# Kernel tuning notes

Hardware: AMD Instinct MI355X
Metric: run time of the kernel (lower is better)

Reference implementation:

```python
import jax, jax.numpy as jnp
import numpy as np

B, S, D = 2, 2048, 1024
NH, NKV = 16, 4
HD = D // NH          # 64
NREP = NH // NKV      # 4
E, TOPK = 8, 2
CAP_FACTOR = 1.25
HID = 4 * D // 3      # 1365 (hardcoded in MoELayer)
EPS = 1e-6


def rmsnorm(x, w):
    xf = x.astype(jnp.float32)
    y = xf * jax.lax.rsqrt(jnp.mean(xf * xf, axis=-1, keepdims=True) + EPS)
    return y.astype(x.dtype) * w


def apply_rope(x, cos, sin):
    # x: [b, s, h, hd]; cos/sin: [1, s, 1, hd]
    half = x.shape[-1] // 2
    x1, x2 = x[..., :half], x[..., half:]
    ch, sh = cos[..., :half], sin[..., :half]
    return jnp.concatenate([x1 * ch - x2 * sh, x1 * sh + x2 * ch], axis=-1)


def swiglu(x, w1, w2, w3):
    return (jax.nn.silu(x @ w1) * (x @ w3)) @ w2


def setup_inputs():
    key = jax.random.key(0)
    ks = jax.random.split(key, 14)
    x = jax.random.normal(ks[0], (B, S, D), jnp.float32)
    # RoPE tables (standard 10000 base), duplicated halves so cos[..., :half] is valid
    pos = jnp.arange(S, dtype=jnp.float32)[:, None]
    inv = 1.0 / (10000.0 ** (jnp.arange(0, HD, 2, dtype=jnp.float32) / HD))  # [HD/2]
    ang = pos * inv[None, :]                                                # [S, HD/2]
    cos = jnp.concatenate([jnp.cos(ang), jnp.cos(ang)], -1)[None, :, None, :]
    sin = jnp.concatenate([jnp.sin(ang), jnp.sin(ang)], -1)[None, :, None, :]
    # causal additive mask [1,1,S,S]
    causal = jnp.tril(jnp.ones((S, S), bool))
    mask = jnp.where(causal, 0.0, -1e9).astype(jnp.float32)[None, None]
    s = 0.02
    return {
        'x': x, 'cos': cos, 'sin': sin, 'mask': mask,
        'attn_norm_w': jnp.ones((D,), jnp.float32),
        'moe_norm_w': jnp.ones((D,), jnp.float32),
        'wq': jax.random.normal(ks[1], (D, NH * HD), jnp.float32) * s,
        'wk': jax.random.normal(ks[2], (D, NKV * HD), jnp.float32) * s,
        'wv': jax.random.normal(ks[3], (D, NKV * HD), jnp.float32) * s,
        'wo': jax.random.normal(ks[4], (NH * HD, D), jnp.float32) * s,
        'router_w': jax.random.normal(ks[5], (D, E), jnp.float32) * s,
        'ew1': jax.random.normal(ks[6], (E, D, HID), jnp.float32) * s,
        'ew2': jax.random.normal(ks[7], (E, HID, D), jnp.float32) * s,
        'ew3': jax.random.normal(ks[8], (E, D, HID), jnp.float32) * s,
        'sw1': jax.random.normal(ks[9], (D, HID), jnp.float32) * s,
        'sw2': jax.random.normal(ks[10], (HID, D), jnp.float32) * s,
        'sw3': jax.random.normal(ks[11], (D, HID), jnp.float32) * s,
    }


def reference(x, cos, sin, mask, attn_norm_w, moe_norm_w, wq, wk, wv, wo,
              router_w, ew1, ew2, ew3, sw1, sw2, sw3):
    # ---- attention path ----
    xn = rmsnorm(x, attn_norm_w)
    q = (xn @ wq).reshape(B, S, NH, HD)
    k = (xn @ wk).reshape(B, S, NKV, HD)
    v = (xn @ wv).reshape(B, S, NKV, HD)
    q = apply_rope(q, cos, sin)
    k = apply_rope(k, cos, sin)
    new_k, new_v = k, v  # kv cache outputs (no prior cache)
    # repeat_interleave kv heads to NH
    k_rep = jnp.repeat(k, NREP, axis=2)  # [b,s,NH,hd]
    v_rep = jnp.repeat(v, NREP, axis=2)
    scores = jnp.einsum('bqhd,bkhd->bhqk', q, k_rep) / np.sqrt(HD)
    scores = scores + mask[:, :, -S:, :]
    attn = jax.nn.softmax(scores.astype(jnp.float32), axis=-1).astype(q.dtype)
    ao = jnp.einsum('bhqk,bkhd->bqhd', attn, v_rep).reshape(B, S, NH * HD)
    h = x + ao @ wo

    # ---- MoE path ----
    hn = rmsnorm(h, moe_norm_w)
    x_flat = hn.reshape(-1, D)            # [T, D]
    T = x_flat.shape[0]
    logits = x_flat @ router_w            # [T, E]
    probs = jax.nn.softmax(logits, axis=-1)
    w_topk, idx = jax.lax.top_k(probs, TOPK)          # [T, K]
    w_topk = w_topk / jnp.sum(w_topk, axis=-1, keepdims=True)
    onehot = jax.nn.one_hot(idx, E, dtype=jnp.float32)  # [T, K, E]
    counts = jnp.sum(onehot, axis=(0, 1))               # [E]
    util = jnp.mean((counts > 0).astype(jnp.float32)) * 100.0
    fraction = counts / T
    aux_loss = E * jnp.sum(jnp.mean(probs, axis=0) * fraction)
    capacity = int(T * TOPK / E * CAP_FACTOR)
    member = jnp.sum(onehot, axis=1) > 0                 # [T, E] token assigned to expert
    keep = member & (jnp.cumsum(member.astype(jnp.int32), axis=0) <= capacity)
    gate = jnp.sum(w_topk[:, :, None] * onehot, axis=1)  # [T, E] combine weights
    gate = gate * keep.astype(gate.dtype)
    # dense per-expert SwiGLU (same math as masked dispatch; zero-gated tokens vanish)
    h1 = jnp.einsum('td,edh->eth', x_flat, ew1)
    h3 = jnp.einsum('td,edh->eth', x_flat, ew3)
    eo = jnp.einsum('eth,ehd->etd', jax.nn.silu(h1) * h3, ew2)
    moe_out = jnp.einsum('etd,te->td', eo, gate).reshape(B, S, D)
    moe_out = moe_out + swiglu(hn, sw1, sw2, sw3)  # shared expert

    out = h + moe_out
    return out, aux_loss, util, new_k, new_v
```

## Files before the change

kernel.cpp:

```cpp
#include <hip/hip_runtime.h>
#include <hip/hip_bf16.h>
#include <math.h>

typedef __hip_bfloat16 bf16;
typedef __attribute__((ext_vector_type(8))) short short8;
typedef __attribute__((ext_vector_type(4))) float floatx4;

#define SEQ    2048
#define TTOK   4096
#define DM     1024
#define NHEAD  16
#define NKVH   4
#define HD     64
#define NEXP   8
#define HIDDEN 1365
#define HIDP   1408
#define CAPT   1280
#define NSLOT  (NEXP*CAPT)
#define TSLOT  (NSLOT+TTOK)
#define XPE    (CAPT/128)
#define XBT    14

__device__ __forceinline__ void gld16(const void* g, void* l) {
  __builtin_amdgcn_global_load_lds((const __attribute__((address_space(1))) void*)g,
                                   (__attribute__((address_space(3))) void*)l,
                                   16, 0, 0);
}

struct __align__(8) bf4 { bf16 x, y, z, w; };

struct EpiAux {
  const float* cosb; const float* sinb;
  bf16* qb; bf16* kb; bf16* vb; float* newk; float* newv;
};

__global__ __launch_bounds__(256) void transpose_cvt(
    const float* __restrict__ src, bf16* __restrict__ dst,
    int K, int N, int Kp, long srcZ, long dstZ) {
  src += (size_t)blockIdx.z * srcZ;
  dst += (size_t)blockIdx.z * dstZ;
  __shared__ float tile[64][65];
  const int tid = threadIdx.x;
  const int k0 = blockIdx.y * 64, n0 = blockIdx.x * 64;
  const int lr = tid >> 4, lc = (tid & 15) * 4;
#pragma unroll
  for (int i = 0; i < 4; ++i) {
    int k = k0 + lr + i * 16;
    int n = n0 + lc;
    float4 v = {0.f, 0.f, 0.f, 0.f};
    if (k < K) {
      if (n + 3 < N) v = *(const float4*)(src + (size_t)k * N + n);
      else {
        float* vp = (float*)&v;
        for (int e = 0; e < 4; ++e) if (n + e < N) vp[e] = src[(size_t)k * N + n + e];
      }
    }
    tile[lr + i * 16][lc] = v.x; tile[lr + i * 16][lc + 1] = v.y;
    tile[lr + i * 16][lc + 2] = v.z; tile[lr + i * 16][lc + 3] = v.w;
  }
  __syncthreads();
  const int n = tid >> 2, kk0 = (tid & 3) * 16;
  if (n0 + n < N) {
    bf16 buf[16];
#pragma unroll
    for (int e = 0; e < 16; ++e) buf[e] = (bf16)tile[kk0 + e][n];
    bf16* dp = dst + (size_t)(n0 + n) * Kp + k0 + kk0;
    *(short8*)dp = *(short8*)buf;
    *(short8*)(dp + 8) = *(short8*)(buf + 8);
  }
}

__global__ __launch_bounds__(256) void rmsnorm_kernel(
    const float* __restrict__ x, const float* __restrict__ w, bf16* __restrict__ out) {
  int t = blockIdx.x;
  const float* xr = x + (size_t)t * DM;
  float4 xv = *(const float4*)(xr + threadIdx.x * 4);
  float ss = xv.x * xv.x + xv.y * xv.y + xv.z * xv.z + xv.w * xv.w;
#pragma unroll
  for (int off = 1; off < 64; off <<= 1) ss += __shfl_xor(ss, off);
  __shared__ float sred[4];
  if ((threadIdx.x & 63) == 0) sred[threadIdx.x >> 6] = ss;
  __syncthreads();
  float scale = rsqrtf((sred[0] + sred[1] + sred[2] + sred[3]) * (1.f / DM) + 1e-6f);
  float4 wv = *(const float4*)(w + threadIdx.x * 4);
  bf4 o;
  o.x = (bf16)(xv.x * scale * wv.x); o.y = (bf16)(xv.y * scale * wv.y);
  o.z = (bf16)(xv.z * scale * wv.z); o.w = (bf16)(xv.w * scale * wv.w);
  ((bf4*)(out + (size_t)t * DM))[threadIdx.x] = o;
}

__global__ __launch_bounds__(256) void rmsnorm_router_kernel(
    const float* __restrict__ x, const float* __restrict__ w, const float* __restrict__ rw,
    bf16* __restrict__ out, float* __restrict__ probs,
    int* __restrict__ tIdx, float* __restrict__ tW) {
  int t = blockIdx.x;
  int tid = threadIdx.x, lane = tid & 63, wv = tid >> 6;
  const float* xr = x + (size_t)t * DM;
  float4 xv = *(const float4*)(xr + tid * 4);
  float ss = xv.x * xv.x + xv.y * xv.y + xv.z * xv.z + xv.w * xv.w;
#pragma unroll
  for (int off = 1; off < 64; off <<= 1) ss += __shfl_xor(ss, off);
  __shared__ float sred[4];
  __shared__ float red[4][8];
  if (lane == 0) sred[wv] = ss;
  __syncthreads();
  float scale = rsqrtf((sred[0] + sred[1] + sred[2] + sred[3]) * (1.f / DM) + 1e-6f);
  float4 wvv = *(const float4*)(w + tid * 4);
  float y[4] = {xv.x * scale * wvv.x, xv.y * scale * wvv.y,
                xv.z * scale * wvv.z, xv.w * scale * wvv.w};
  bf4 o; o.x = (bf16)y[0]; o.y = (bf16)y[1]; o.z = (bf16)y[2]; o.w = (bf16)y[3];
  ((bf4*)(out + (size_t)t * DM))[tid] = o;
  float acc[8] = {0, 0, 0, 0, 0, 0, 0, 0};
#pragma unroll
  for (int dd = 0; dd < 4; ++dd) {
    const float* rwr = rw + (size_t)(tid * 4 + dd) * 8;
#pragma unroll
    for (int e = 0; e < 8; ++e) acc[e] += y[dd] * rwr[e];
  }
#pragma unroll
  for (int e = 0; e < 8; ++e)
#pragma unroll
    for (int off = 1; off < 64; off <<= 1) acc[e] += __shfl_xor(acc[e], off);
  if (lane == 0)
#pragma unroll
    for (int e = 0; e < 8; ++e) red[wv][e] = acc[e];
  __syncthreads();
  if (tid == 0) {
    float lg[8];
#pragma unroll
    for (int e = 0; e < 8; ++e) lg[e] = red[0][e] + red[1][e] + red[2][e] + red[3][e];
    float mx = lg[0];
#pragma unroll
    for (int e = 1; e < 8; ++e) mx = fmaxf(mx, lg[e]);
    float p[8], se = 0.f;
#pragma unroll
    for (int e = 0; e < 8; ++e) { p[e] = __expf(lg[e] - mx); se += p[e]; }
#pragma unroll
    for (int e = 0; e < 8; ++e) { p[e] /= se; probs[t * 8 + e] = p[e]; }
    int i1 = 0;
#pragma unroll
    for (int e = 1; e < 8; ++e) if (p[e] > p[i1]) i1 = e;
    int i2 = (i1 == 0) ? 1 : 0;
#pragma unroll
    for (int e = 0; e < 8; ++e) if (e != i1 && p[e] > p[i2]) i2 = e;
    float s = p[i1] + p[i2];
    tIdx[t * 2] = i1; tIdx[t * 2 + 1] = i2;
    tW[t * 2] = p[i1] / s; tW[t * 2 + 1] = p[i2] / s;
  }
}

template <int EPI>
__global__ __launch_bounds__(256) void gemm_bt(
    const bf16* __restrict__ A, const bf16* __restrict__ Bt,
    int M, int N, int K, int lda, int ldb, int xPerXcd,
    float* __restrict__ Cf, int ldc,
    const float* __restrict__ resid, EpiAux aux) {
  __shared__ __align__(16) bf16 As[64 * 64];
  __shared__ __align__(16) bf16 Bs[128 * 64];
  const int tid = threadIdx.x, lane = tid & 63, wave = tid >> 6;
  const int f = blockIdx.x, lo = f >> 3;
  int xb = (f & 7) * xPerXcd + lo % xPerXcd;
  int n0 = (lo / xPerXcd) * 128;
  int m0 = xb * 64;

  const bf16* aSrc[2]; const bf16* bSrc[4];
  bf16* aDst[2]; bf16* bDst[4];
#pragma unroll
  for (int it = 0; it < 2; ++it) {
    int c = it * 256 + tid;
    int r = c >> 3, q = c & 7;
    int kq = q ^ (r & 7);
    aSrc[it] = A + (long)(m0 + r) * lda + kq * 8;
    aDst[it] = As + (size_t)(it * 256 + wave * 64) * 8;
  }
#pragma unroll
  for (int it = 0; it < 4; ++it) {
    int c = it * 256 + tid;
    int r = c >> 3, q = c & 7;
    int kq = q ^ (r & 7);
    bSrc[it] = Bt + (long)(n0 + r) * ldb + kq * 8;
    bDst[it] = Bs + (size_t)(it * 256 + wave * 64) * 8;
  }

  floatx4 acc[2][4];
#pragma unroll
  for (int i = 0; i < 2; ++i)
#pragma unroll
    for (int j = 0; j < 4; ++j) { floatx4 z = {0.f, 0.f, 0.f, 0.f}; acc[i][j] = z; }

  const int wm = (wave & 1) * 32, wn = (wave >> 1) * 64;
  const int l15 = lane & 15, quad = lane >> 4;
  int aOff[2][2], bOff[4][2];
#pragma unroll
  for (int h = 0; h < 2; ++h) {
#pragma unroll
    for (int i = 0; i < 2; ++i) {
      int m = wm + i * 16 + l15;
      aOff[i][h] = (((m << 3) | ((h * 4 + quad) ^ (m & 7))) << 3);
    }
#pragma unroll
    for (int j = 0; j < 4; ++j) {
      int n = wn + j * 16 + l15;
      bOff[j][h] = (((n << 3) | ((h * 4 + quad) ^ (n & 7))) << 3);
    }
  }

  const int kIters = K >> 6;
  for (int kt = 0; kt < kIters; ++kt) {
    __syncthreads();
#pragma unroll
    for (int it = 0; it < 2; ++it) { gld16(aSrc[it], aDst[it]); aSrc[it] += 64; }
#pragma unroll
    for (int it = 0; it < 4; ++it) { gld16(bSrc[it], bDst[it]); bSrc[it] += 64; }
    __syncthreads();
#pragma unroll
    for (int h = 0; h < 2; ++h) {
      short8 af[2], bfr[4];
#pragma unroll
      for (int i = 0; i < 2; ++i) af[i] = *(const short8*)(As + aOff[i][h]);
#pragma unroll
      for (int j = 0; j < 4; ++j) bfr[j] = *(const short8*)(Bs + bOff[j][h]);
#pragma unroll
      for (int i = 0; i < 2; ++i)
#pragma unroll
        for (int j = 0; j < 4; ++j)
          acc[i][j] = __builtin_amdgcn_mfma_f32_16x16x32_bf16(af[i], bfr[j], acc[i][j], 0, 0, 0);
    }
  }

  if constexpr (EPI == 4) {
#pragma unroll
    for (int i = 0; i < 2; ++i) {
#pragma unroll
      for (int r = 0; r < 4; ++r) {
        int row = wm + i * 16 + quad * 4 + r;
        int t = m0 + row;
        int s = t & (SEQ - 1);
        if (n0 < 1024) {
#pragma unroll
          for (int j = 0; j < 2; ++j) {
            int col = n0 + wn + j * 16 + l15;
            int dlo = col & 63;
            float x1 = acc[i][j][r], x2 = acc[i][j + 2][r];
            float ch = aux.cosb[s * 64 + dlo], sh = aux.sinb[s * 64 + dlo];
            aux.qb[(size_t)t * DM + col]      = (bf16)((x1 * ch - x2 * sh) * 0.125f);
            aux.qb[(size_t)t * DM + col + 32] = (bf16)((x1 * sh + x2 * ch) * 0.125f);
          }
        } else if (n0 < 1280) {
#pragma unroll
          for (int j = 0; j < 2; ++j) {
            int ck = n0 + wn + j * 16 + l15 - 1024;
            int dlo = ck & 63;
            float x1 = acc[i][j][r], x2 = acc[i][j + 2][r];
            float ch = aux.cosb[s * 64 + dlo], sh = aux.sinb[s * 64 + dlo];
            float o1 = x1 * ch - x2 * sh, o2 = x1 * sh + x2 * ch;
            aux.kb[(size_t)t * 256 + ck]        = (bf16)o1;
            aux.kb[(size_t)t * 256 + ck + 32]   = (bf16)o2;
            aux.newk[(size_t)t * 256 + ck]      = o1;
            aux.newk[(size_t)t * 256 + ck + 32] = o2;
          }
        } else {
#pragma unroll
          for (int j = 0; j < 4; ++j) {
            int cv = n0 + wn + j * 16 + l15 - 1280;
            float v = acc[i][j][r];
            aux.vb[(size_t)t * 256 + cv]   = (bf16)v;
            aux.newv[(size_t)t * 256 + cv] = v;
          }
        }
      }
    }
    return;
  }
#pragma unroll
  for (int i = 0; i < 2; ++i) {
#pragma unroll
    for (int j = 0; j < 4; ++j) {
      int col = n0 + wn + j * 16 + l15;
#pragma unroll
      for (int r = 0; r < 4; ++r) {
        int row = wm + i * 16 + quad * 4 + r;
        size_t o = (size_t)(m0 + row) * ldc + col;
        Cf[o] = resid[o] + acc[i][j][r];
      }
    }
  }
}

__device__ __forceinline__ bool slot_block(
    int f, int NY, const int* neCnt, int& expert, int& m0, int& mLimit, int& n0) {
  int xcd = f & 7, lo = f >> 3;
  int xb = lo / NY, y = lo % NY;
  n0 = y * 64;
  if (xb < XPE) {
    expert = xcd;
    int ne = neCnt[xcd];
    if (xb * 128 >= ne) return false;
    m0 = xcd * CAPT + xb * 128;
    mLimit = ne - xb * 128;
    if (mLimit > 128) mLimit = 128;
  } else {
    expert = 8;
    int sb = xcd * 4 + (xb - XPE);
    m0 = NSLOT + sb * 128;
    mLimit = 128;
  }
  return true;
}

__global__ __launch_bounds__(256, 2) void gemm_dual9(
    const bf16* __restrict__ A, const bf16* __restrict__ B1t, const bf16* __restrict__ B3t,
    bf16* __restrict__ mact,
    const int* __restrict__ tokList, const int* __restrict__ neCnt) {
  __shared__ __align__(16) bf16 As[128 * 64];
  __shared__ __align__(16) bf16 B1s[128 * 64];
  __shared__ __align__(16) bf16 B3s[128 * 64];
  const int tid = threadIdx.x, lane = tid & 63, wave = tid >> 6;
  int expert, m0, mLimit, n0;
  if (!slot_block(blockIdx.x, 11, neCnt, expert, m0, mLimit, n0)) return;
  n0 <<= 1;
  const bf16* B1e = B1t + (long)expert * (HIDDEN * 1024);
  const bf16* B3e = B3t + (long)expert * (HIDDEN * 1024);

  const bf16* aSrc[4]; const bf16* b1Src[4]; const bf16* b3Src[4];
  bf16* aDst[4]; bf16* b1Dst[4]; bf16* b3Dst[4];
#pragma unroll
  for (int it = 0; it < 4; ++it) {
    int c = it * 256 + tid;
    int r = c >> 3, q = c & 7;
    int kq = q ^ (r & 7);
    int rr = r < mLimit ? r : (mLimit - 1);
    aSrc[it] = A + (long)tokList[m0 + rr] * 1024 + kq * 8;
    aDst[it] = As + (size_t)(it * 256 + wave * 64) * 8;
    int nn = n0 + r; if (nn > HIDDEN - 1) nn = HIDDEN - 1;
    b1Src[it] = B1e + (long)nn * 1024 + kq * 8;
    b3Src[it] = B3e + (long)nn * 1024 + kq * 8;
    b1Dst[it] = B1s + (size_t)(it * 256 + wave * 64) * 8;
    b3Dst[it] = B3s + (size_t)(it * 256 + wave * 64) * 8;
  }

  floatx4 acc1[4][4], acc3[4][4];
#pragma unroll
  for (int i = 0; i < 4; ++i)
#pragma unroll
    for (int j = 0; j < 4; ++j) {
      floatx4 z = {0.f, 0.f, 0.f, 0.f};
      acc1[i][j] = z; acc3[i][j] = z;
    }

  const int wm = (wave & 1) * 64, wn = (wave >> 1) * 64;
  const int l15 = lane & 15, quad = lane >> 4;
  int aOff[4][2], bOff[4][2];
#pragma unroll
  for (int h = 0; h < 2; ++h) {
#pragma unroll
    for (int i = 0; i < 4; ++i) {
      int m = wm + i * 16 + l15;
      aOff[i][h] = (((m << 3) | ((h * 4 + quad) ^ (m & 7))) << 3);
    }
#pragma unroll
    for (int j = 0; j < 4; ++j) {
      int n = wn + j * 16 + l15;
      bOff[j][h] = (((n << 3) | ((h * 4 + quad) ^ (n & 7))) << 3);
    }
  }

  for (int kt = 0; kt < 16; ++kt) {
    __syncthreads();
#pragma unroll
    for (int it = 0; it < 4; ++it) { gld16(aSrc[it], aDst[it]); aSrc[it] += 64; }
#pragma unroll
    for (int it = 0; it < 4; ++it) {
      gld16(b1Src[it], b1Dst[it]); b1Src[it] += 64;
      gld16(b3Src[it], b3Dst[it]); b3Src[it] += 64;
    }
    __syncthreads();
#pragma unroll
    for (int h = 0; h < 2; ++h) {
      short8 af[4];
#pragma unroll
      for (int i = 0; i < 4; ++i) af[i] = *(const short8*)(As + aOff[i][h]);
#pragma unroll
      for (int j = 0; j < 4; ++j) {
        short8 b1f = *(const short8*)(B1s + bOff[j][h]);
        short8 b3f = *(const short8*)(B3s + bOff[j][h]);
#pragma unroll
        for (int i = 0; i < 4; ++i) {
          acc1[i][j] = __builtin_amdgcn_mfma_f32_16x16x32_bf16(af[i], b1f, acc1[i][j], 0, 0, 0);
          acc3[i][j] = __builtin_amdgcn_mfma_f32_16x16x32_bf16(af[i], b3f, acc3[i][j], 0, 0, 0);
        }
      }
    }
  }

#pragma unroll
  for (int i = 0; i < 4; ++i) {
#pragma unroll
    for (int j = 0; j < 4; ++j) {
      int col = n0 + wn + j * 16 + l15;
#pragma unroll
      for (int r = 0; r < 4; ++r) {
        int row = wm + i * 16 + quad * 4 + r;
        if (row >= mLimit) continue;
        float a1 = acc1[i][j][r], a3 = acc3[i][j][r];
        float sl = a1 / (1.f + __expf(-a1));
        mact[(size_t)(m0 + row) * HIDP + col] = (col < HIDDEN) ? (bf16)(sl * a3) : (bf16)0.f;
      }
    }
  }
}

__global__ __launch_bounds__(256) void gemm_down9(
    const bf16* __restrict__ A, const bf16* __restrict__ B2t,
    bf16* __restrict__ eo,
    const float* __restrict__ gateW, const int* __restrict__ neCnt) {
  __shared__ __align__(16) bf16 As[128 * 64];
  __shared__ __align__(16) bf16 Bs[64 * 64];
  const int tid = threadIdx.x, lane = tid & 63, wave = tid >> 6;
  int expert, m0, mLimit, n0;
  if (!slot_block(blockIdx.x, 16, neCnt, expert, m0, mLimit, n0)) return;
  const bf16* Be = B2t + (long)expert * (1024 * HIDP);

  const bf16* aSrc[4]; const bf16* bSrc[2];
  bf16* aDst[4]; bf16* bDst[2];
#pragma unroll
  for (int it = 0; it < 4; ++it) {
    int c = it * 256 + tid;
    int r = c >> 3, q = c & 7;
    int kq = q ^ (r & 7);
    int rr = r < mLimit ? r : (mLimit - 1);
    aSrc[it] = A + (long)(m0 + rr) * HIDP + kq * 8;
    aDst[it] = As + (size_t)(it * 256 + wave * 64) * 8;
  }
#pragma unroll
  for (int it = 0; it < 2; ++it) {
    int c = it * 256 + tid;
    int r = c >> 3, q = c & 7;
    int kq = q ^ (r & 7);
    bSrc[it] = Be + (long)(n0 + r) * HIDP + kq * 8;
    bDst[it] = Bs + (size_t)(it * 256 + wave * 64) * 8;
  }

  floatx4 acc[4][2];
#pragma unroll
  for (int i = 0; i < 4; ++i)
#pragma unroll
    for (int j = 0; j < 2; ++j) { floatx4 z = {0.f, 0.f, 0.f, 0.f}; acc[i][j] = z; }

  const int wm = (wave & 1) * 64, wn = (wave >> 1) * 32;
  const int l15 = lane & 15, quad = lane >> 4;
  int aOff[4][2], bOff[2][2];
#pragma unroll
  for (int h = 0; h < 2; ++h) {
#pragma unroll
    for (int i = 0; i < 4; ++i) {
      int m = wm + i * 16 + l15;
      aOff[i][h] = (((m << 3) | ((h * 4 + quad) ^ (m & 7))) << 3);
    }
#pragma unroll
    for (int j = 0; j < 2; ++j) {
      int n = wn + j * 16 + l15;
      bOff[j][h] = (((n << 3) | ((h * 4 + quad) ^ (n & 7))) << 3);
    }
  }

  for (int kt = 0; kt < 22; ++kt) {
    __syncthreads();
#pragma unroll
    for (int it = 0; it < 4; ++it) { gld16(aSrc[it], aDst[it]); aSrc[it] += 64; }
#pragma unroll
    for (int it = 0; it < 2; ++it) { gld16(bSrc[it], bDst[it]); bSrc[it] += 64; }
    __syncthreads();
#pragma unroll
    for (int h = 0; h < 2; ++h) {
      short8 af[4];
#pragma unroll
      for (int i = 0; i < 4; ++i) af[i] = *(const short8*)(As + aOff[i][h]);
#pragma unroll
      for (int j = 0; j < 2; ++j) {
        short8 bf = *(const short8*)(Bs + bOff[j][h]);
#pragma unroll
        for (int i = 0; i < 4; ++i)
          acc[i][j] = __builtin_amdgcn_mfma_f32_16x16x32_bf16(af[i], bf, acc[i][j], 0, 0, 0);
      }
    }
  }

#pragma unroll
  for (int i = 0; i < 4; ++i) {
#pragma unroll
    for (int j = 0; j < 2; ++j) {
      int col = n0 + wn + j * 16 + l15;
#pragma unroll
      for (int r = 0; r < 4; ++r) {
        int row = wm + i * 16 + quad * 4 + r;
        if (row >= mLimit) continue;
        eo[(size_t)(m0 + row) * 1024 + col] = (bf16)(gateW[m0 + row] * acc[i][j][r]);
      }
    }
  }
}

__global__ __launch_bounds__(256) void vt_kernel(
    const bf16* __restrict__ vb, bf16* __restrict__ vt) {
  __shared__ __align__(16) bf16 tile[64 * 72];
  int t0 = blockIdx.x * 64, bg = blockIdx.y;
  int b = bg >> 2, g = bg & 3;
  int tid = threadIdx.x;
  for (int c = tid; c < 512; c += 256) {
    int r = c >> 3, d8 = (c & 7) * 8;
    *(short8*)(tile + r * 72 + d8) =
        *(const short8*)(vb + (size_t)(b * SEQ + t0 + r) * 256 + g * 64 + d8);
  }
  __syncthreads();
  for (int c = tid; c < 512; c += 256) {
    int d = c >> 3, s8 = (c & 7) * 8;
    bf16 tmp[8];
#pragma unroll
    for (int x = 0; x < 8; ++x) tmp[x] = tile[(s8 + x) * 72 + d];
    *(short8*)(vt + ((size_t)bg * 64 + d) * SEQ + t0 + s8) = *(short8*)tmp;
  }
}

__global__ __launch_bounds__(256) void attn_kernel(
    const bf16* __restrict__ Q, const bf16* __restrict__ Kc, const bf16* __restrict__ Vt,
    bf16* __restrict__ AO) {
  __shared__ __align__(16) bf16 Qs[64 * 64];
  __shared__ __align__(16) bf16 Ks[64 * 64];
  __shared__ __align__(16) bf16 Vs[64 * 64];
  __shared__ __align__(16) bf16 Ps[4][16 * 64];
  const int pairI = blockIdx.x, h = blockIdx.y, b = blockIdx.z;
  const int g = h >> 2;
  const int tid = threadIdx.x, lane = tid & 63, wave = tid >> 6;
  const int l15 = lane & 15, quad = lane >> 4;

  const bf16* kSrc[2]; const bf16* vSrc[2]; bf16* kDst[2]; bf16* vDst[2];
#pragma unroll
  for (int it = 0; it < 2; ++it) {
    int c = it * 256 + tid;
    int r = c >> 3, p = c & 7;
    int kq = p ^ (r & 7);
    kSrc[it] = Kc + (size_t)(b * SEQ + r) * 256 + g * 64 + kq * 8;
    vSrc[it] = Vt + ((size_t)(b * 4 + g) * 64 + r) * SEQ + kq * 8;
    kDst[it] = Ks + (size_t)(it * 256 + wave * 64) * 8;
    vDst[it] = Vs + (size_t)(it * 256 + wave * 64) * 8;
  }

  int qOff[2], kvOff[4][2], pOff[2];
#pragma unroll
  for (int hh = 0; hh < 2; ++hh) {
    int m = wave * 16 + l15;
    qOff[hh] = (m << 6) + (((hh * 4 + quad) ^ (m & 7)) << 3);
#pragma unroll
    for (int j = 0; j < 4; ++j) {
      int n = j * 16 + l15;
      kvOff[j][hh] = (n << 6) + (((hh * 4 + quad) ^ (n & 7)) << 3);
    }
    int cblk = (hh * 2 + (quad >> 1)) ^ (l15 >> 2);
    pOff[hh] = (l15 << 6) + (cblk << 4) + ((quad & 1) << 3);
  }
  bf16* pw = &Ps[wave][0];
  const int rowl = wave * 16 + quad * 4;

  short8 onesb;
#pragma unroll
  for (int e = 0; e < 8; ++e) onesb[e] = (short)0x3F80;

  for (int ph = 0; ph < 2; ++ph) {
    const int q0 = (ph == 0 ? pairI : 31 - pairI) * 64;
    __syncthreads();
#pragma unroll
    for (int it = 0; it < 2; ++it) {
      int c = it * 256 + tid;
      int r = c >> 3, p = c & 7;
      int kq = p ^ (r & 7);
      gld16(Q + (size_t)(b * SEQ + q0 + r) * DM + h * 64 + kq * 8,
            Qs + (size_t)(it * 256 + wave * 64) * 8);
    }

    floatx4 oacc[4], sumacc;
#pragma unroll
    for (int r = 0; r < 4; ++r) { floatx4 z = {0.f, 0.f, 0.f, 0.f}; oacc[r] = z; }
    { floatx4 z = {0.f, 0.f, 0.f, 0.f}; sumacc = z; }

    const int nkt = (q0 >> 6) + 1;
    for (int kt = 0; kt < nkt; ++kt) {
      __syncthreads();
#pragma unroll
      for (int it = 0; it < 2; ++it) {
        gld16(kSrc[it] + (size_t)kt * 64 * 256, kDst[it]);
        gld16(vSrc[it] + kt * 64, vDst[it]);
      }
      __syncthreads();

      floatx4 sacc[4];
#pragma unroll
      for (int j = 0; j < 4; ++j) { floatx4 z = {0.f, 0.f, 0.f, 0.f}; sacc[j] = z; }
#pragma unroll
      for (int hh = 0; hh < 2; ++hh) {
        short8 aq = *(const short8*)(Qs + qOff[hh]);
#pragma unroll
        for (int j = 0; j < 4; ++j)
          sacc[j] = __builtin_amdgcn_mfma_f32_16x16x32_bf16(
              aq, *(const short8*)(Ks + kvOff[j][hh]), sacc[j], 0, 0, 0);
      }

      const bool lastTile = (kt == nkt - 1);
#pragma unroll
      for (int j = 0; j < 4; ++j) {
        int sw = ((j ^ quad) << 4) + l15;
        int colg = j * 16 + l15;
#pragma unroll
        for (int r = 0; r < 4; ++r) {
          float p = __expf(sacc[j][r]);
          if (lastTile && colg > rowl + r) p = 0.f;
          pw[(quad * 4 + r) * 64 + sw] = (bf16)p;
        }
      }
      asm volatile("s_waitcnt lgkmcnt(0)" ::: "memory");
#pragma unroll
      for (int hh = 0; hh < 2; ++hh) {
        short8 ap = *(const short8*)(pw + pOff[hh]);
#pragma unroll
        for (int j = 0; j < 4; ++j)
          oacc[j] = __builtin_amdgcn_mfma_f32_16x16x32_bf16(
              ap, *(const short8*)(Vs + kvOff[j][hh]), oacc[j], 0, 0, 0);
        sumacc = __builtin_amdgcn_mfma_f32_16x16x32_bf16(ap, onesb, sumacc, 0, 0, 0);
      }
    }

    float inv[4];
#pragma unroll
    for (int r = 0; r < 4; ++r) inv[r] = 1.f / sumacc[r];
#pragma unroll
    for (int j = 0; j < 4; ++j)
#pragma unroll
      for (int r = 0; r < 4; ++r) {
        int t = b * SEQ + q0 + rowl + r;
        AO[(size_t)t * DM + h * 64 + j * 16 + l15] = (bf16)(oacc[j][r] * inv[r]);
      }
  }
}

__global__ __launch_bounds__(256) void assign_kernel(
    const int* __restrict__ tIdx, const float* __restrict__ tW,
    int* __restrict__ tokList, float* __restrict__ gateW,
    int* __restrict__ neCnt, int* __restrict__ cntFull, int* __restrict__ slotOf) {
  int e = blockIdx.x;
  int tid = threadIdx.x, lane = tid & 63, wv = tid >> 6;
  if (e == 8) {
    for (int t = tid; t < TTOK; t += 256) {
      tokList[NSLOT + t] = t;
      gateW[NSLOT + t] = 1.0f;
    }
    if (tid == 0) neCnt[8] = TTOK;
    return;
  }
  __shared__ int waveTot[4];
  __shared__ int offs;
  if (tid == 0) offs = 0;
  __syncthreads();
  for (int base = 0; base < TTOK; base += 256) {
    int t = base + tid;
    int a = tIdx[t * 2], b2 = tIdx[t * 2 + 1];
    bool sel = (a == e) || (b2 == e);
    unsigned long long mask = __ballot(sel);
    int wrank = __popcll(mask & ((1ull << lane) - 1ull));
    if (lane == 0) waveTot[wv] = __popcll(mask);
    __syncthreads();
    int pre = offs;
    for (int w2 = 0; w2 < wv; ++w2) pre += waveTot[w2];
    int rank = pre + wrank;
    if (sel && rank < CAPT) {
      int slot = e * CAPT + rank;
      tokList[slot] = t;
      gateW[slot] = (a == e) ? tW[t * 2] : tW[t * 2 + 1];
      slotOf[t * 2 + ((a == e) ? 0 : 1)] = slot;
    }
    __syncthreads();
    if (tid == 0) offs += waveTot[0] + waveTot[1] + waveTot[2] + waveTot[3];
    __syncthreads();
  }
  if (tid == 0) {
    cntFull[e] = offs;
    neCnt[e] = offs < CAPT ? offs : CAPT;
  }
}

__global__ __launch_bounds__(256) void aux_kernel(
    const float* __restrict__ probs, const int* __restrict__ cntFull,
    float* __restrict__ outAux) {
  __shared__ float psum[8];
  if (threadIdx.x < 8) psum[threadIdx.x] = 0.f;
  __syncthreads();
  float lp[8] = {0, 0, 0, 0, 0, 0, 0, 0};
  for (int t = threadIdx.x; t < TTOK; t += 256) {
#pragma unroll
    for (int e = 0; e < 8; ++e) lp[e] += probs[t * 8 + e];
  }
#pragma unroll
  for (int e = 0; e < 8; ++e)
#pragma unroll
    for (int off = 1; off < 64; off <<= 1) lp[e] += __shfl_xor(lp[e], off);
  if ((threadIdx.x & 63) == 0)
#pragma unroll
    for (int e = 0; e < 8; ++e) atomicAdd(&psum[e], lp[e]);
  __syncthreads();
  if (threadIdx.x == 0) {
    float aux = 0.f; int used = 0;
    for (int e = 0; e < 8; ++e) {
      aux += (psum[e] / (float)TTOK) * ((float)cntFull[e] / (float)TTOK);
      if (cntFull[e] > 0) used++;
    }
    outAux[0] = 8.f * aux;
    outAux[1] = 100.f * (float)used / 8.f;
  }
}

__global__ __launch_bounds__(256) void combine_kernel(
    float* __restrict__ outp, const float* __restrict__ hbuf,
    const bf16* __restrict__ eo, const int* __restrict__ slotOf) {
  int t = blockIdx.x, tid = threadIdx.x;
  float4 v = ((const float4*)(hbuf + (size_t)t * DM))[tid];
  bf4 sh = ((const bf4*)(eo + (size_t)(NSLOT + t) * DM))[tid];
  v.x += (float)sh.x; v.y += (float)sh.y; v.z += (float)sh.z; v.w += (float)sh.w;
  int s0 = slotOf[t * 2], s1 = slotOf[t * 2 + 1];
  if (s0 >= 0) {
    bf4 e = ((const bf4*)(eo + (size_t)s0 * DM))[tid];
    v.x += (float)e.x; v.y += (float)e.y; v.z += (float)e.z; v.w += (float)e.w;
  }
  if (s1 >= 0) {
    bf4 e = ((const bf4*)(eo + (size_t)s1 * DM))[tid];
    v.x += (float)e.x; v.y += (float)e.y; v.z += (float)e.z; v.w += (float)e.w;
  }
  ((float4*)(outp + (size_t)t * DM))[tid] = v;
}

extern "C" void kernel_launch(void* const* d_in, const int* in_sizes, int n_in,
                              void* d_out, int out_size, void* d_ws, size_t ws_size,
                              hipStream_t stream) {
  (void)in_sizes; (void)n_in; (void)out_size; (void)ws_size;
  const float* x     = (const float*)d_in[0];
  const float* cosb  = (const float*)d_in[1];
  const float* sinb  = (const float*)d_in[2];
  const float* attnw = (const float*)d_in[4];
  const float* moew  = (const float*)d_in[5];
  const float* wq  = (const float*)d_in[6];
  const float* wk  = (const float*)d_in[7];
  const float* wv  = (const float*)d_in[8];
  const float* wo  = (const float*)d_in[9];
  const float* rw  = (const float*)d_in[10];
  const float* ew1 = (const float*)d_in[11];
  const float* ew2 = (const float*)d_in[12];
  const float* ew3 = (const float*)d_in[13];
  const float* sw1 = (const float*)d_in[14];
  const float* sw2 = (const float*)d_in[15];
  const float* sw3 = (const float*)d_in[16];

  float* outp = (float*)d_out;
  float* auxp = outp + 4194304;
  float* newk = outp + 4194306;
  float* newv = newk + 1048576;

  char* wsp = (char*)d_ws;
  size_t off = 0;
  auto alloc = [&](size_t bytes) -> void* {
    void* p = wsp + off; off += (bytes + 255) & ~(size_t)255; return p;
  };
  bf16* wqkvT = (bf16*)alloc((size_t)1536 * 1024 * 2);
  bf16* woT   = (bf16*)alloc((size_t)1024 * 1024 * 2);
  bf16* ew1T  = (bf16*)alloc((size_t)9 * HIDDEN * 1024 * 2);
  bf16* ew3T  = (bf16*)alloc((size_t)9 * HIDDEN * 1024 * 2);
  bf16* ew2T  = (bf16*)alloc((size_t)9 * 1024 * HIDP * 2);
  bf16* xn    = (bf16*)alloc((size_t)TTOK * DM * 2);
  bf16* qb    = (bf16*)alloc((size_t)TTOK * DM * 2);
  bf16* kb    = (bf16*)alloc((size_t)TTOK * 256 * 2);
  bf16* vb    = (bf16*)alloc((size_t)TTOK * 256 * 2);
  bf16* vt    = (bf16*)alloc((size_t)TTOK * 256 * 2);
  bf16* ao    = (bf16*)alloc((size_t)TTOK * DM * 2);
  float* hbuf = (float*)alloc((size_t)TTOK * DM * 4);
  bf16* hn    = (bf16*)alloc((size_t)TTOK * DM * 2);
  float* probs = (float*)alloc((size_t)TTOK * 8 * 4);
  int*   tIdx  = (int*)alloc((size_t)TTOK * 2 * 4);
  float* tW    = (float*)alloc((size_t)TTOK * 2 * 4);
  int*   tokList = (int*)alloc((size_t)TSLOT * 4);
  float* gateW   = (float*)alloc((size_t)TSLOT * 4);
  int*   neCnt   = (int*)alloc(64);
  int*   cntFull = (int*)alloc(64);
  int*   slotOf  = (int*)alloc((size_t)TTOK * 2 * 4);
  bf16*  mact = (bf16*)alloc((size_t)TSLOT * HIDP * 2);
  bf16*  eo   = (bf16*)alloc((size_t)TSLOT * DM * 2);

  EpiAux nil{};
  EpiAux ropeAux{cosb, sinb, qb, kb, vb, newk, newv};

  transpose_cvt<<<dim3(16, 16, 1), 256, 0, stream>>>(wq, wqkvT, 1024, 1024, 1024, 0, 0);
  transpose_cvt<<<dim3(4, 16, 1), 256, 0, stream>>>(wk, wqkvT + (size_t)1024 * 1024, 1024, 256, 1024, 0, 0);
  transpose_cvt<<<dim3(4, 16, 1), 256, 0, stream>>>(wv, wqkvT + (size_t)1280 * 1024, 1024, 256, 1024, 0, 0);
  transpose_cvt<<<dim3(16, 16, 1), 256, 0, stream>>>(wo, woT, 1024, 1024, 1024, 0, 0);
  transpose_cvt<<<dim3(22, 16, NEXP), 256, 0, stream>>>(ew1, ew1T, 1024, HIDDEN, 1024,
      (long)1024 * HIDDEN, (long)HIDDEN * 1024);
  transpose_cvt<<<dim3(22, 16, NEXP), 256, 0, stream>>>(ew3, ew3T, 1024, HIDDEN, 1024,
      (long)1024 * HIDDEN, (long)HIDDEN * 1024);
  transpose_cvt<<<dim3(16, 22, NEXP), 256, 0, stream>>>(ew2, ew2T, HIDDEN, 1024, HIDP,
      (long)HIDDEN * 1024, (long)1024 * HIDP);
  transpose_cvt<<<dim3(22, 16, 1), 256, 0, stream>>>(sw1, ew1T + (size_t)8 * HIDDEN * 1024,
      1024, HIDDEN, 1024, 0, 0);
  transpose_cvt<<<dim3(22, 16, 1), 256, 0, stream>>>(sw3, ew3T + (size_t)8 * HIDDEN * 1024,
      1024, HIDDEN, 1024, 0, 0);
  transpose_cvt<<<dim3(16, 22, 1), 256, 0, stream>>>(sw2, ew2T + (size_t)8 * 1024 * HIDP,
      HIDDEN, 1024, HIDP, 0, 0);

  rmsnorm_kernel<<<TTOK, 256, 0, stream>>>(x, attnw, xn);
  gemm_bt<4><<<8 * 8 * 12, 256, 0, stream>>>(
      xn, wqkvT, TTOK, 1536, 1024, 1024, 1024, 8, nullptr, 0, nullptr, ropeAux);
  vt_kernel<<<dim3(32, 8), 256, 0, stream>>>(vb, vt);
  attn_kernel<<<dim3(16, NHEAD, 2), 256, 0, stream>>>(qb, kb, vt, ao);
  gemm_bt<2><<<8 * 8 * 8, 256, 0, stream>>>(
      ao, woT, TTOK, 1024, 1024, 1024, 1024, 8, hbuf, 1024, x, nil);

  rmsnorm_router_kernel<<<TTOK, 256, 0, stream>>>(hbuf, moew, rw, hn, probs, tIdx, tW);
  hipMemsetAsync(slotOf, 0xFF, (size_t)TTOK * 2 * 4, stream);
  assign_kernel<<<9, 256, 0, stream>>>(tIdx, tW, tokList, gateW, neCnt, cntFull, slotOf);
  aux_kernel<<<1, 256, 0, stream>>>(probs, cntFull, auxp);

  gemm_dual9<<<8 * XBT * 11, 256, 0, stream>>>(hn, ew1T, ew3T, mact, tokList, neCnt);
  gemm_down9<<<8 * XBT * 16, 256, 0, stream>>>(mact, ew2T, eo, gateW, neCnt);
  combine_kernel<<<TTOK, 256, 0, stream>>>(outp, hbuf, eo, slotOf);
}
```

Before: 560.9 us.

## Fuse MoE combine into down-projection via atomic scatter-add; unpair attention query tiles

The down-projection GEMM now scatters gate-weighted results straight into the output with float atomicAdd, keyed by each slot's token. The output projection writes the residual sum into the output buffer as well. This removes the eo intermediate buffer, the slotOf map with its memset, and the combine kernel. Separately, attention launches one block per 64-row query tile, heaviest first, instead of pairing a light and a heavy tile in one block. Atomics make the summation order nondeterministic and add contention on the output.

```diff
diff --git a/kernel.cpp b/kernel.cpp
--- a/kernel.cpp
+++ b/kernel.cpp
@@ -154,7 +154,7 @@
     const bf16* __restrict__ A, const bf16* __restrict__ Bt,
     int M, int N, int K, int lda, int ldb, int xPerXcd,
     float* __restrict__ Cf, int ldc,
-    const float* __restrict__ resid, EpiAux aux) {
+    const float* __restrict__ resid, float* __restrict__ out2, EpiAux aux) {
   __shared__ __align__(16) bf16 As[64 * 64];
   __shared__ __align__(16) bf16 Bs[128 * 64];
   const int tid = threadIdx.x, lane = tid & 63, wave = tid >> 6;
@@ -281,7 +281,9 @@
       for (int r = 0; r < 4; ++r) {
         int row = wm + i * 16 + quad * 4 + r;
         size_t o = (size_t)(m0 + row) * ldc + col;
-        Cf[o] = resid[o] + acc[i][j][r];
+        float v = resid[o] + acc[i][j][r];
+        Cf[o] = v;
+        out2[o] = v;
       }
     }
   }
@@ -412,8 +414,9 @@
 
 __global__ __launch_bounds__(256) void gemm_down9(
     const bf16* __restrict__ A, const bf16* __restrict__ B2t,
-    bf16* __restrict__ eo,
-    const float* __restrict__ gateW, const int* __restrict__ neCnt) {
+    float* __restrict__ outp,
+    const float* __restrict__ gateW, const int* __restrict__ tokList,
+    const int* __restrict__ neCnt) {
   __shared__ __align__(16) bf16 As[128 * 64];
   __shared__ __align__(16) bf16 Bs[64 * 64];
   const int tid = threadIdx.x, lane = tid & 63, wave = tid >> 6;
@@ -489,13 +492,16 @@
 #pragma unroll
   for (int i = 0; i < 4; ++i) {
 #pragma unroll
-    for (int j = 0; j < 2; ++j) {
-      int col = n0 + wn + j * 16 + l15;
-#pragma unroll
-      for (int r = 0; r < 4; ++r) {
-        int row = wm + i * 16 + quad * 4 + r;
-        if (row >= mLimit) continue;
-        eo[(size_t)(m0 + row) * 1024 + col] = (bf16)(gateW[m0 + row] * acc[i][j][r]);
+    for (int r = 0; r < 4; ++r) {
+      int row = wm + i * 16 + quad * 4 + r;
+      if (row >= mLimit) continue;
+      int slot = m0 + row;
+      int tok = tokList[slot];
+      float gw = gateW[slot];
+#pragma unroll
+      for (int j = 0; j < 2; ++j) {
+        int col = n0 + wn + j * 16 + l15;
+        atomicAdd(outp + (size_t)tok * 1024 + col, gw * acc[i][j][r]);
       }
     }
   }
@@ -529,7 +535,8 @@
   __shared__ __align__(16) bf16 Ks[64 * 64];
   __shared__ __align__(16) bf16 Vs[64 * 64];
   __shared__ __align__(16) bf16 Ps[4][16 * 64];
-  const int pairI = blockIdx.x, h = blockIdx.y, b = blockIdx.z;
+  const int h = blockIdx.y, b = blockIdx.z;
+  const int q0 = (31 - blockIdx.x) * 64;
   const int g = h >> 2;
   const int tid = threadIdx.x, lane = tid & 63, wave = tid >> 6;
   const int l15 = lane & 15, quad = lane >> 4;
@@ -566,86 +573,82 @@
 #pragma unroll
   for (int e = 0; e < 8; ++e) onesb[e] = (short)0x3F80;
 
-  for (int ph = 0; ph < 2; ++ph) {
-    const int q0 = (ph == 0 ? pairI : 31 - pairI) * 64;
+#pragma unroll
+  for (int it = 0; it < 2; ++it) {
+    int c = it * 256 + tid;
+    int r = c >> 3, p = c & 7;
+    int kq = p ^ (r & 7);
+    gld16(Q + (size_t)(b * SEQ + q0 + r) * DM + h * 64 + kq * 8,
+          Qs + (size_t)(it * 256 + wave * 64) * 8);
+  }
+
+  floatx4 oacc[4], sumacc;
+#pragma unroll
+  for (int r = 0; r < 4; ++r) { floatx4 z = {0.f, 0.f, 0.f, 0.f}; oacc[r] = z; }
+  { floatx4 z = {0.f, 0.f, 0.f, 0.f}; sumacc = z; }
+
+  const int nkt = (q0 >> 6) + 1;
+  for (int kt = 0; kt < nkt; ++kt) {
     __syncthreads();
 #pragma unroll
     for (int it = 0; it < 2; ++it) {
-      int c = it * 256 + tid;
-      int r = c >> 3, p = c & 7;
-      int kq = p ^ (r & 7);
-      gld16(Q + (size_t)(b * SEQ + q0 + r) * DM + h * 64 + kq * 8,
-            Qs + (size_t)(it * 256 + wave * 64) * 8);
-    }
-
-    floatx4 oacc[4], sumacc;
-#pragma unroll
-    for (int r = 0; r < 4; ++r) { floatx4 z = {0.f, 0.f, 0.f, 0.f}; oacc[r] = z; }
-    { floatx4 z = {0.f, 0.f, 0.f, 0.f}; sumacc = z; }
-
-    const int nkt = (q0 >> 6) + 1;
-    for (int kt = 0; kt < nkt; ++kt) {
-      __syncthreads();
-#pragma unroll
-      for (int it = 0; it < 2; ++it) {
-        gld16(kSrc[it] + (size_t)kt * 64 * 256, kDst[it]);
-        gld16(vSrc[it] + kt * 64, vDst[it]);
+      gld16(kSrc[it] + (size_t)kt * 64 * 256, kDst[it]);
+      gld16(vSrc[it] + kt * 64, vDst[it]);
+    }
+    __syncthreads();
+
+    floatx4 sacc[4];
+#pragma unroll
+    for (int j = 0; j < 4; ++j) { floatx4 z = {0.f, 0.f, 0.f, 0.f}; sacc[j] = z; }
+#pragma unroll
+    for (int hh = 0; hh < 2; ++hh) {
+      short8 aq = *(const short8*)(Qs + qOff[hh]);
+#pragma unroll
+      for (int j = 0; j < 4; ++j)
+        sacc[j] = __builtin_amdgcn_mfma_f32_16x16x32_bf16(
+            aq, *(const short8*)(Ks + kvOff[j][hh]), sacc[j], 0, 0, 0);
+    }
+
+    const bool lastTile = (kt == nkt - 1);
+#pragma unroll
+    for (int j = 0; j < 4; ++j) {
+      int sw = ((j ^ quad) << 4) + l15;
+      int colg = j * 16 + l15;
+#pragma unroll
+      for (int r = 0; r < 4; ++r) {
+        float p = __expf(sacc[j][r]);
+        if (lastTile && colg > rowl + r) p = 0.f;
+        pw[(quad * 4 + r) * 64 + sw] = (bf16)p;
       }
-      __syncthreads();
-
-      floatx4 sacc[4];
-#pragma unroll
-      for (int j = 0; j < 4; ++j) { floatx4 z = {0.f, 0.f, 0.f, 0.f}; sacc[j] = z; }
-#pragma unroll
-      for (int hh = 0; hh < 2; ++hh) {
-        short8 aq = *(const short8*)(Qs + qOff[hh]);
-#pragma unroll
-        for (int j = 0; j < 4; ++j)
-          sacc[j] = __builtin_amdgcn_mfma_f32_16x16x32_bf16(
-              aq, *(const short8*)(Ks + kvOff[j][hh]), sacc[j], 0, 0, 0);
-      }
-
-      const bool lastTile = (kt == nkt - 1);
-#pragma unroll
-      for (int j = 0; j < 4; ++j) {
-        int sw = ((j ^ quad) << 4) + l15;
-        int colg = j * 16 + l15;
-#pragma unroll
-        for (int r = 0; r < 4; ++r) {
-          float p = __expf(sacc[j][r]);
-          if (lastTile && colg > rowl + r) p = 0.f;
-          pw[(quad * 4 + r) * 64 + sw] = (bf16)p;
-        }
-      }
-      asm volatile("s_waitcnt lgkmcnt(0)" ::: "memory");
-#pragma unroll
-      for (int hh = 0; hh < 2; ++hh) {
-        short8 ap = *(const short8*)(pw + pOff[hh]);
-#pragma unroll
-        for (int j = 0; j < 4; ++j)
-          oacc[j] = __builtin_amdgcn_mfma_f32_16x16x32_bf16(
-              ap, *(const short8*)(Vs + kvOff[j][hh]), oacc[j], 0, 0, 0);
-        sumacc = __builtin_amdgcn_mfma_f32_16x16x32_bf16(ap, onesb, sumacc, 0, 0, 0);
-      }
-    }
-
-    float inv[4];
-#pragma unroll
-    for (int r = 0; r < 4; ++r) inv[r] = 1.f / sumacc[r];
-#pragma unroll
-    for (int j = 0; j < 4; ++j)
-#pragma unroll
-      for (int r = 0; r < 4; ++r) {
-        int t = b * SEQ + q0 + rowl + r;
-        AO[(size_t)t * DM + h * 64 + j * 16 + l15] = (bf16)(oacc[j][r] * inv[r]);
-      }
-  }
+    }
+    asm volatile("s_waitcnt lgkmcnt(0)" ::: "memory");
+#pragma unroll
+    for (int hh = 0; hh < 2; ++hh) {
+      short8 ap = *(const short8*)(pw + pOff[hh]);
+#pragma unroll
+      for (int j = 0; j < 4; ++j)
+        oacc[j] = __builtin_amdgcn_mfma_f32_16x16x32_bf16(
+            ap, *(const short8*)(Vs + kvOff[j][hh]), oacc[j], 0, 0, 0);
+      sumacc = __builtin_amdgcn_mfma_f32_16x16x32_bf16(ap, onesb, sumacc, 0, 0, 0);
+    }
+  }
+
+  float inv[4];
+#pragma unroll
+  for (int r = 0; r < 4; ++r) inv[r] = 1.f / sumacc[r];
+#pragma unroll
+  for (int j = 0; j < 4; ++j)
+#pragma unroll
+    for (int r = 0; r < 4; ++r) {
+      int t = b * SEQ + q0 + rowl + r;
+      AO[(size_t)t * DM + h * 64 + j * 16 + l15] = (bf16)(oacc[j][r] * inv[r]);
+    }
 }
 
 __global__ __launch_bounds__(256) void assign_kernel(
     const int* __restrict__ tIdx, const float* __restrict__ tW,
     int* __restrict__ tokList, float* __restrict__ gateW,
-    int* __restrict__ neCnt, int* __restrict__ cntFull, int* __restrict__ slotOf) {
+    int* __restrict__ neCnt, int* __restrict__ cntFull) {
   int e = blockIdx.x;
   int tid = threadIdx.x, lane = tid & 63, wv = tid >> 6;
   if (e == 8) {
@@ -675,7 +678,6 @@
       int slot = e * CAPT + rank;
       tokList[slot] = t;
       gateW[slot] = (a == e) ? tW[t * 2] : tW[t * 2 + 1];
-      slotOf[t * 2 + ((a == e) ? 0 : 1)] = slot;
     }
     __syncthreads();
     if (tid == 0) offs += waveTot[0] + waveTot[1] + waveTot[2] + waveTot[3];
@@ -715,25 +717,6 @@
     outAux[0] = 8.f * aux;
     outAux[1] = 100.f * (float)used / 8.f;
   }
-}
-
-__global__ __launch_bounds__(256) void combine_kernel(
-    float* __restrict__ outp, const float* __restrict__ hbuf,
-    const bf16* __restrict__ eo, const int* __restrict__ slotOf) {
-  int t = blockIdx.x, tid = threadIdx.x;
-  float4 v = ((const float4*)(hbuf + (size_t)t * DM))[tid];
-  bf4 sh = ((const bf4*)(eo + (size_t)(NSLOT + t) * DM))[tid];
-  v.x += (float)sh.x; v.y += (float)sh.y; v.z += (float)sh.z; v.w += (float)sh.w;
-  int s0 = slotOf[t * 2], s1 = slotOf[t * 2 + 1];
-  if (s0 >= 0) {
-    bf4 e = ((const bf4*)(eo + (size_t)s0 * DM))[tid];
-    v.x += (float)e.x; v.y += (float)e.y; v.z += (float)e.z; v.w += (float)e.w;
-  }
-  if (s1 >= 0) {
-    bf4 e = ((const bf4*)(eo + (size_t)s1 * DM))[tid];
-    v.x += (float)e.x; v.y += (float)e.y; v.z += (float)e.z; v.w += (float)e.w;
-  }
-  ((float4*)(outp + (size_t)t * DM))[tid] = v;
 }
 
 extern "C" void kernel_launch(void* const* d_in, const int* in_sizes, int n_in,
@@ -787,9 +770,7 @@
   float* gateW   = (float*)alloc((size_t)TSLOT * 4);
   int*   neCnt   = (int*)alloc(64);
   int*   cntFull = (int*)alloc(64);
-  int*   slotOf  = (int*)alloc((size_t)TTOK * 2 * 4);
   bf16*  mact = (bf16*)alloc((size_t)TSLOT * HIDP * 2);
-  bf16*  eo   = (bf16*)alloc((size_t)TSLOT * DM * 2);
 
   EpiAux nil{};
   EpiAux ropeAux{cosb, sinb, qb, kb, vb, newk, newv};
@@ -813,18 +794,16 @@
 
   rmsnorm_kernel<<<TTOK, 256, 0, stream>>>(x, attnw, xn);
   gemm_bt<4><<<8 * 8 * 12, 256, 0, stream>>>(
-      xn, wqkvT, TTOK, 1536, 1024, 1024, 1024, 8, nullptr, 0, nullptr, ropeAux);
+      xn, wqkvT, TTOK, 1536, 1024, 1024, 1024, 8, nullptr, 0, nullptr, nullptr, ropeAux);
   vt_kernel<<<dim3(32, 8), 256, 0, stream>>>(vb, vt);
-  attn_kernel<<<dim3(16, NHEAD, 2), 256, 0, stream>>>(qb, kb, vt, ao);
+  attn_kernel<<<dim3(32, NHEAD, 2), 256, 0, stream>>>(qb, kb, vt, ao);
   gemm_bt<2><<<8 * 8 * 8, 256, 0, stream>>>(
-      ao, woT, TTOK, 1024, 1024, 1024, 1024, 8, hbuf, 1024, x, nil);
+      ao, woT, TTOK, 1024, 1024, 1024, 1024, 8, hbuf, 1024, x, outp, nil);
 
   rmsnorm_router_kernel<<<TTOK, 256, 0, stream>>>(hbuf, moew, rw, hn, probs, tIdx, tW);
-  hipMemsetAsync(slotOf, 0xFF, (size_t)TTOK * 2 * 4, stream);
-  assign_kernel<<<9, 256, 0, stream>>>(tIdx, tW, tokList, gateW, neCnt, cntFull, slotOf);
+  assign_kernel<<<9, 256, 0, stream>>>(tIdx, tW, tokList, gateW, neCnt, cntFull);
   aux_kernel<<<1, 256, 0, stream>>>(probs, cntFull, auxp);
 
   gemm_dual9<<<8 * XBT * 11, 256, 0, stream>>>(hn, ew1T, ew3T, mact, tokList, neCnt);
-  gemm_down9<<<8 * XBT * 16, 256, 0, stream>>>(mact, ew2T, eo, gateW, neCnt);
-  combine_kernel<<<TTOK, 256, 0, stream>>>(outp, hbuf, eo, slotOf);
-}
+  gemm_down9<<<8 * XBT * 16, 256, 0, stream>>>(mact, ew2T, outp, gateW, tokList, neCnt);
+}
```

New measurement: 593.8 us. 5.9% more time.
